# Optimization experiments

Hardware: AMD Instinct MI355X
Metric: run time of the kernel (lower is better)

## Reference

```python
import jax, jax.numpy as jnp
import numpy as np

EPS = 1e-12
TOPK = 6

def _l2norm(x):
    # matches torch F.normalize(p=2, eps=1e-12)
    n = jnp.linalg.norm(x, axis=-1, keepdims=True)
    return x / jnp.maximum(n, EPS)

def setup_inputs() -> dict:
    key = jax.random.key(0)
    k1, k2 = jax.random.split(key)
    nC, M, P, d = 5, 512, 196, 384
    support = jax.random.normal(k1, (nC, P, d), dtype=jnp.float32)
    query = jax.random.normal(k2, (M, P, d), dtype=jnp.float32)
    scale_cls = jnp.full((1,), 10.0, dtype=jnp.float32)  # init value in module
    bias = jnp.zeros((1,), dtype=jnp.float32)
    return {"support": support, "query": query, "scale_cls": scale_cls, "bias": bias}

def reference(support, query, scale_cls, bias):
    q = _l2norm(query)      # [M, P, d]
    s = _l2norm(support)    # [nC, P, d]
    # batched cosine similarity between every query patch and support patch
    sim = jnp.einsum('mpd,cqd->mcpq', q, s)   # [M, nC, P, P]
    # max over support patches, then sum of top-6 query-patch matches
    m = sim.max(axis=3)                        # [M, nC, P]
    top6 = jax.lax.top_k(m, TOPK)[0].sum(axis=-1)  # [M, nC]
    cls_scores = top6[None]                    # [1, M, nC] (unsqueeze(0))
    return scale_cls * (cls_scores + bias)
```

## Files before the change

### kernel.cpp

```cpp
#include <hip/hip_runtime.h>
#include <hip/hip_bf16.h>
#include <cstdint>

typedef __attribute__((ext_vector_type(8))) short short8;
typedef __attribute__((ext_vector_type(4))) float floatx4;

#define NC   5
#define PP   196
#define DD   384
#define MM   512
#define ROWS (MM * PP)
#define NRB  1568
#define EPSN 1e-12f
#define ASTR 392

#define TILE_BYTES  49152
#define KSTEP_BYTES 4096

__device__ __forceinline__ unsigned enc_f(float f) {
    unsigned u = __float_as_uint(f);
    return (u & 0x80000000u) ? ~u : (u | 0x80000000u);
}
__device__ __forceinline__ float dec_f(unsigned u) {
    unsigned b = (u & 0x80000000u) ? (u ^ 0x80000000u) : ~u;
    return __uint_as_float(b);
}
#define ENC_NEG_INF 0x007FFFFFu

__global__ __launch_bounds__(256) void k_norm0(const float* __restrict__ sup,
                                               float* __restrict__ sinv) {
    int wid = threadIdx.x >> 6, lane = threadIdx.x & 63;
    int r = blockIdx.x * 4 + wid;
    if (r >= NC * PP) return;
    const float* src = sup + (size_t)r * DD;
    float s = 0.f;
    #pragma unroll
    for (int j = 0; j < 6; ++j) { float v = src[lane + j * 64]; s += v * v; }
    #pragma unroll
    for (int off = 1; off < 64; off <<= 1) s += __shfl_xor(s, off, 64);
    if (lane == 0) sinv[r] = 1.0f / fmaxf(sqrtf(s), EPSN);
}

__global__ __launch_bounds__(256) void k_swz(const float* __restrict__ sup,
                                             const float* __restrict__ sinv,
                                             __hip_bfloat16* __restrict__ snw) {
    int s = blockIdx.x * 256 + threadIdx.x;
    int lane = s & 63;
    int r1 = s >> 6;
    int ct = r1 & 3;
    int r2 = r1 >> 2;
    int kk = r2 % 12;
    int g  = r2 / 12;
    int c = g >> 2, t = g & 3;
    int c16 = lane & 15, quad = lane >> 4;
    int cl = t * 64 + ct * 16 + c16;
    if (cl > PP - 1) cl = PP - 1;
    int srow = c * PP + cl;
    const float* sp = sup + (size_t)srow * DD + kk * 32 + quad * 8;
    float inv = sinv[srow];
    alignas(16) __hip_bfloat16 hb[8];
    #pragma unroll
    for (int e = 0; e < 8; ++e) hb[e] = __float2bfloat16(sp[e] * inv);
    *(uint4*)((char*)snw + (size_t)s * 16) = *(const uint4*)hb;
}

__global__ __launch_bounds__(256, 3) void k_gemm_max(const float* __restrict__ q,
                                                     const __hip_bfloat16* __restrict__ snw,
                                                     float* __restrict__ rowmaxg) {
    __shared__ __hip_bfloat16 As[64 * ASTR];
    __shared__ unsigned rmax[64 * NC];
    __shared__ float rss[64];

    const int tid  = threadIdx.x;
    const int row0 = blockIdx.x * 64;
    const int lane = tid & 63;
    const int wav  = tid >> 6;
    const int quad = lane >> 4, c16 = lane & 15;

    for (int i = tid; i < 64 * NC; i += 256) rmax[i] = ENC_NEG_INF;

    {
        const int arow = tid >> 2;
        const int asub = tid & 3;
        const float* src = q + (size_t)(row0 + arow) * DD;
        float ss = 0.f;
        #pragma unroll
        for (int i = 0; i < 12; ++i) {
            int ch = asub + i * 4;
            const floatx4* p = (const floatx4*)(src + ch * 8);
            floatx4 x0 = __builtin_nontemporal_load(p);
            floatx4 x1 = __builtin_nontemporal_load(p + 1);
            ss += x0.x*x0.x + x0.y*x0.y + x0.z*x0.z + x0.w*x0.w
                + x1.x*x1.x + x1.y*x1.y + x1.z*x1.z + x1.w*x1.w;
            alignas(16) __hip_bfloat16 hb[8];
            hb[0] = __float2bfloat16(x0.x); hb[1] = __float2bfloat16(x0.y);
            hb[2] = __float2bfloat16(x0.z); hb[3] = __float2bfloat16(x0.w);
            hb[4] = __float2bfloat16(x1.x); hb[5] = __float2bfloat16(x1.y);
            hb[6] = __float2bfloat16(x1.z); hb[7] = __float2bfloat16(x1.w);
            *(uint4*)&As[arow * ASTR + ch * 8] = *(const uint4*)hb;
        }
        ss += __shfl_xor(ss, 1, 64);
        ss += __shfl_xor(ss, 2, 64);
        if (asub == 0) rss[arow] = ss;
    }
    __syncthreads();

    #pragma unroll 1
    for (int g = wav; g < 20; g += 4) {
        floatx4 acc[4][4];
        #pragma unroll
        for (int i = 0; i < 4; ++i)
            #pragma unroll
            for (int j = 0; j < 4; ++j) acc[i][j] = (floatx4){0.f, 0.f, 0.f, 0.f};

        const char* bbase = (const char*)snw + (size_t)g * TILE_BYTES + (size_t)lane * 16;
        short8 b0[4], b1[4], a[4];
        #pragma unroll
        for (int ct = 0; ct < 4; ++ct) b0[ct] = ((const short8*)bbase)[ct * 64];

        #pragma unroll 1
        for (int kk = 0; kk < 12; kk += 2) {
            #pragma unroll
            for (int ct = 0; ct < 4; ++ct)
                b1[ct] = ((const short8*)(bbase + (kk + 1) * KSTEP_BYTES))[ct * 64];
            #pragma unroll
            for (int rt = 0; rt < 4; ++rt)
                a[rt] = *(const short8*)&As[(rt * 16 + c16) * ASTR + kk * 32 + quad * 8];
            #pragma unroll
            for (int rt = 0; rt < 4; ++rt)
                #pragma unroll
                for (int ct = 0; ct < 4; ++ct)
                    acc[rt][ct] = __builtin_amdgcn_mfma_f32_16x16x32_bf16(
                        a[rt], b0[ct], acc[rt][ct], 0, 0, 0);
            if (kk + 2 < 12) {
                #pragma unroll
                for (int ct = 0; ct < 4; ++ct)
                    b0[ct] = ((const short8*)(bbase + (kk + 2) * KSTEP_BYTES))[ct * 64];
            }
            #pragma unroll
            for (int rt = 0; rt < 4; ++rt)
                a[rt] = *(const short8*)&As[(rt * 16 + c16) * ASTR + (kk + 1) * 32 + quad * 8];
            #pragma unroll
            for (int rt = 0; rt < 4; ++rt)
                #pragma unroll
                for (int ct = 0; ct < 4; ++ct)
                    acc[rt][ct] = __builtin_amdgcn_mfma_f32_16x16x32_bf16(
                        a[rt], b1[ct], acc[rt][ct], 0, 0, 0);
        }

        const int c = g >> 2;
        #pragma unroll
        for (int rt = 0; rt < 4; ++rt) {
            #pragma unroll
            for (int reg = 0; reg < 4; ++reg) {
                float mx = fmaxf(fmaxf(acc[rt][0][reg], acc[rt][1][reg]),
                                 fmaxf(acc[rt][2][reg], acc[rt][3][reg]));
                #pragma unroll
                for (int off = 1; off < 16; off <<= 1)
                    mx = fmaxf(mx, __shfl_xor(mx, off, 64));
                if (c16 == 0) {
                    int rloc = rt * 16 + quad * 4 + reg;
                    atomicMax(&rmax[rloc * NC + c], enc_f(mx));
                }
            }
        }
    }

    __syncthreads();
    for (int i = tid; i < 64 * NC; i += 256) {
        int row = i / NC, c = i % NC;
        float inv = 1.0f / fmaxf(sqrtf(rss[row]), EPSN);
        __builtin_nontemporal_store(dec_f(rmax[row * NC + c]) * inv,
                                    &rowmaxg[(size_t)(row0 + row) * NC + c]);
    }
}

__global__ __launch_bounds__(256) void k_top6(const float* __restrict__ rowmaxg,
                                              const float* __restrict__ scale,
                                              const float* __restrict__ bias,
                                              float* __restrict__ out) {
    int wav = threadIdx.x >> 6, lane = threadIdx.x & 63;
    int pair = blockIdx.x * 4 + wav;
    if (pair >= MM * NC) return;
    int m = pair / NC, c = pair % NC;
    size_t base = (size_t)m * PP;
    float v[4];
    #pragma unroll
    for (int i = 0; i < 4; ++i) {
        int p = lane + i * 64;
        v[i] = (p < PP) ? rowmaxg[(base + p) * NC + c] : -INFINITY;
    }
    float sum = 0.f;
    for (int t = 0; t < 6; ++t) {
        float bv = v[0]; int bi = 0;
        #pragma unroll
        for (int i = 1; i < 4; ++i) { if (v[i] > bv) { bv = v[i]; bi = i; } }
        int gid = bi * 64 + lane;
        #pragma unroll
        for (int off = 1; off < 64; off <<= 1) {
            float ov = __shfl_xor(bv, off, 64);
            int og  = __shfl_xor(gid, off, 64);
            if (ov > bv || (ov == bv && og < gid)) { bv = ov; gid = og; }
        }
        sum += bv;
        if ((gid & 63) == lane) v[gid >> 6] = -INFINITY;
    }
    if (lane == 0) out[pair] = scale[0] * (sum + bias[0]);
}

extern "C" void kernel_launch(void* const* d_in, const int* in_sizes, int n_in,
                              void* d_out, int out_size, void* d_ws, size_t ws_size,
                              hipStream_t stream) {
    const float* support = (const float*)d_in[0];
    const float* query   = (const float*)d_in[1];
    const float* scale   = (const float*)d_in[2];
    const float* bias    = (const float*)d_in[3];
    float* out = (float*)d_out;

    char* ws = (char*)d_ws;
    __hip_bfloat16* snw = (__hip_bfloat16*)ws;
    float* sinv         = (float*)(ws + 983040);
    float* rowmaxg      = (float*)(ws + 983040 + 4096);

    hipLaunchKernelGGL(k_norm0,   dim3(245),  dim3(256), 0, stream, support, sinv);
    hipLaunchKernelGGL(k_swz,     dim3(240),  dim3(256), 0, stream, support, sinv, snw);
    hipLaunchKernelGGL(k_gemm_max,dim3(NRB),  dim3(256), 0, stream, query, snw, rowmaxg);
    hipLaunchKernelGGL(k_top6,    dim3(640),  dim3(256), 0, stream, rowmaxg, scale, bias, out);
}
```

Baseline: 326.1 us.

## Swizzle A tile into MFMA fragment order, triple-buffer B loads, transpose rowmax layout

The query tile in shared memory is now stored in the exact MFMA fragment order, so each lane reads a contiguous 16-byte chunk indexed by lane instead of a padded row-stride layout. The B-operand register prefetch becomes a three-deep pipeline that also prefetches the next group's tile across the group loop boundary, which keeps MFMAs fed. The intermediate rowmax buffer is transposed to class-major order, so the top-6 kernel reads it coalesced. The changes cost extra registers for the third B buffer and make the code more complex.

```diff
diff --git a/kernel.cpp b/kernel.cpp
--- a/kernel.cpp
+++ b/kernel.cpp
@@ -12,7 +12,6 @@
 #define ROWS (MM * PP)
 #define NRB  1568
 #define EPSN 1e-12f
-#define ASTR 392
 
 #define TILE_BYTES  49152
 #define KSTEP_BYTES 4096
@@ -67,7 +66,7 @@
 __global__ __launch_bounds__(256, 3) void k_gemm_max(const float* __restrict__ q,
                                                      const __hip_bfloat16* __restrict__ snw,
                                                      float* __restrict__ rowmaxg) {
-    __shared__ __hip_bfloat16 As[64 * ASTR];
+    __shared__ __hip_bfloat16 As[12 * 4 * 64 * 8];
     __shared__ unsigned rmax[64 * NC];
     __shared__ float rss[64];
 
@@ -75,13 +74,13 @@
     const int row0 = blockIdx.x * 64;
     const int lane = tid & 63;
     const int wav  = tid >> 6;
-    const int quad = lane >> 4, c16 = lane & 15;
 
     for (int i = tid; i < 64 * NC; i += 256) rmax[i] = ENC_NEG_INF;
 
     {
         const int arow = tid >> 2;
         const int asub = tid & 3;
+        const int rt   = arow >> 4, c16 = arow & 15;
         const float* src = q + (size_t)(row0 + arow) * DD;
         float ss = 0.f;
         #pragma unroll
@@ -97,7 +96,8 @@
             hb[2] = __float2bfloat16(x0.z); hb[3] = __float2bfloat16(x0.w);
             hb[4] = __float2bfloat16(x1.x); hb[5] = __float2bfloat16(x1.y);
             hb[6] = __float2bfloat16(x1.z); hb[7] = __float2bfloat16(x1.w);
-            *(uint4*)&As[arow * ASTR + ch * 8] = *(const uint4*)hb;
+            int kk = ch >> 2, quad = ch & 3;
+            *(uint4*)&As[(((kk * 4 + rt) * 64) + quad * 16 + c16) * 8] = *(const uint4*)hb;
         }
         ss += __shfl_xor(ss, 1, 64);
         ss += __shfl_xor(ss, 2, 64);
@@ -105,6 +105,43 @@
     }
     __syncthreads();
 
+    const char* bbase = (const char*)snw + (size_t)wav * TILE_BYTES + (size_t)lane * 16;
+    short8 b0[4], b1[4], b2[4], a[4];
+    #pragma unroll
+    for (int ct = 0; ct < 4; ++ct) b0[ct] = ((const short8*)(bbase + 0 * KSTEP_BYTES))[ct * 64];
+    #pragma unroll
+    for (int ct = 0; ct < 4; ++ct) b1[ct] = ((const short8*)(bbase + 1 * KSTEP_BYTES))[ct * 64];
+    #pragma unroll
+    for (int ct = 0; ct < 4; ++ct) b2[ct] = ((const short8*)(bbase + 2 * KSTEP_BYTES))[ct * 64];
+
+    #define LOAD_NEXT(buf, step)                                                     \
+        do {                                                                         \
+            int nk = kk + 3 + (step);                                                \
+            if (nk < 12) {                                                           \
+                _Pragma("unroll")                                                    \
+                for (int ct = 0; ct < 4; ++ct)                                       \
+                    buf[ct] = ((const short8*)(bbase + nk * KSTEP_BYTES))[ct * 64];  \
+            } else if (g + 4 < 20) {                                                 \
+                _Pragma("unroll")                                                    \
+                for (int ct = 0; ct < 4; ++ct)                                       \
+                    buf[ct] = ((const short8*)(bbase + 4 * TILE_BYTES +              \
+                                               (nk - 12) * KSTEP_BYTES))[ct * 64];   \
+            }                                                                        \
+        } while (0)
+
+    #define MFMA_STEP(buf, kkoff)                                                    \
+        do {                                                                         \
+            _Pragma("unroll")                                                        \
+            for (int rt = 0; rt < 4; ++rt)                                           \
+                a[rt] = *(const short8*)&As[(((kk + (kkoff)) * 4 + rt) * 64 + lane) * 8]; \
+            _Pragma("unroll")                                                        \
+            for (int rt = 0; rt < 4; ++rt)                                           \
+                _Pragma("unroll")                                                    \
+                for (int ct = 0; ct < 4; ++ct)                                       \
+                    acc[rt][ct] = __builtin_amdgcn_mfma_f32_16x16x32_bf16(           \
+                        a[rt], buf[ct], acc[rt][ct], 0, 0, 0);                       \
+        } while (0)
+
     #pragma unroll 1
     for (int g = wav; g < 20; g += 4) {
         floatx4 acc[4][4];
@@ -113,42 +150,15 @@
             #pragma unroll
             for (int j = 0; j < 4; ++j) acc[i][j] = (floatx4){0.f, 0.f, 0.f, 0.f};
 
-        const char* bbase = (const char*)snw + (size_t)g * TILE_BYTES + (size_t)lane * 16;
-        short8 b0[4], b1[4], a[4];
-        #pragma unroll
-        for (int ct = 0; ct < 4; ++ct) b0[ct] = ((const short8*)bbase)[ct * 64];
-
         #pragma unroll 1
-        for (int kk = 0; kk < 12; kk += 2) {
-            #pragma unroll
-            for (int ct = 0; ct < 4; ++ct)
-                b1[ct] = ((const short8*)(bbase + (kk + 1) * KSTEP_BYTES))[ct * 64];
-            #pragma unroll
-            for (int rt = 0; rt < 4; ++rt)
-                a[rt] = *(const short8*)&As[(rt * 16 + c16) * ASTR + kk * 32 + quad * 8];
-            #pragma unroll
-            for (int rt = 0; rt < 4; ++rt)
-                #pragma unroll
-                for (int ct = 0; ct < 4; ++ct)
-                    acc[rt][ct] = __builtin_amdgcn_mfma_f32_16x16x32_bf16(
-                        a[rt], b0[ct], acc[rt][ct], 0, 0, 0);
-            if (kk + 2 < 12) {
-                #pragma unroll
-                for (int ct = 0; ct < 4; ++ct)
-                    b0[ct] = ((const short8*)(bbase + (kk + 2) * KSTEP_BYTES))[ct * 64];
-            }
-            #pragma unroll
-            for (int rt = 0; rt < 4; ++rt)
-                a[rt] = *(const short8*)&As[(rt * 16 + c16) * ASTR + (kk + 1) * 32 + quad * 8];
-            #pragma unroll
-            for (int rt = 0; rt < 4; ++rt)
-                #pragma unroll
-                for (int ct = 0; ct < 4; ++ct)
-                    acc[rt][ct] = __builtin_amdgcn_mfma_f32_16x16x32_bf16(
-                        a[rt], b1[ct], acc[rt][ct], 0, 0, 0);
+        for (int kk = 0; kk < 12; kk += 3) {
+            MFMA_STEP(b0, 0); LOAD_NEXT(b0, 0);
+            MFMA_STEP(b1, 1); LOAD_NEXT(b1, 1);
+            MFMA_STEP(b2, 2); LOAD_NEXT(b2, 2);
         }
 
         const int c = g >> 2;
+        const int quad = lane >> 4, c16 = lane & 15;
         #pragma unroll
         for (int rt = 0; rt < 4; ++rt) {
             #pragma unroll
@@ -164,14 +174,15 @@
                 }
             }
         }
+        bbase += 4 * TILE_BYTES;
     }
 
     __syncthreads();
     for (int i = tid; i < 64 * NC; i += 256) {
-        int row = i / NC, c = i % NC;
+        int c = i >> 6, row = i & 63;
         float inv = 1.0f / fmaxf(sqrtf(rss[row]), EPSN);
         __builtin_nontemporal_store(dec_f(rmax[row * NC + c]) * inv,
-                                    &rowmaxg[(size_t)(row0 + row) * NC + c]);
+                                    &rowmaxg[(size_t)c * ROWS + row0 + row]);
     }
 }
 
@@ -183,12 +194,12 @@
     int pair = blockIdx.x * 4 + wav;
     if (pair >= MM * NC) return;
     int m = pair / NC, c = pair % NC;
-    size_t base = (size_t)m * PP;
+    size_t base = (size_t)c * ROWS + (size_t)m * PP;
     float v[4];
     #pragma unroll
     for (int i = 0; i < 4; ++i) {
         int p = lane + i * 64;
-        v[i] = (p < PP) ? rowmaxg[(base + p) * NC + c] : -INFINITY;
+        v[i] = (p < PP) ? rowmaxg[base + p] : -INFINITY;
     }
     float sum = 0.f;
     for (int t = 0; t < 6; ++t) {
```

New measurement: 323.6 us. No clear change (-0.8%).
